# Kernel optimization log

Hardware: AMD Instinct MI355X
Metric: run time of the kernel (lower is better)

Reference implementation:

```python
import jax, jax.numpy as jnp
import numpy as np

HEADS = 16
DIM_HEAD = 64

def setup_inputs() -> dict:
    key = jax.random.key(0)
    ks = jax.random.split(key, 5)
    B, S, D = 2, 2048, 1024
    return {
        "hidden_states": jax.random.normal(ks[0], (B, S, D), dtype=jnp.float32),
        "Wq": jax.random.normal(ks[1], (D, D), dtype=jnp.float32) * (D ** -0.5),
        "Wkv": jax.random.normal(ks[2], (D, D), dtype=jnp.float32) * (D ** -0.5),
        "Wout": jax.random.normal(ks[3], (D, D), dtype=jnp.float32) * (D ** -0.5),
        "bout": jnp.zeros((D,), dtype=jnp.float32),
    }

def reference(hidden_states, Wq, Wkv, Wout, bout):
    B, S, D = hidden_states.shape
    H, Dh = HEADS, DIM_HEAD
    # projections (torch Linear: x @ W.T; here weights are stored as [in, out])
    q = hidden_states @ Wq            # [B, S, D]
    kv = hidden_states @ Wkv          # key == value share the to_kv projection
    q = q.reshape(B, S, H, Dh).transpose(0, 2, 1, 3)   # [B, H, S, Dh]
    k = kv.reshape(B, S, H, Dh).transpose(0, 2, 1, 3)
    v = k
    scale = 1.0 / np.sqrt(Dh).astype(np.float32)
    # ReLU attention: no softmax
    attn = jax.nn.relu(jnp.einsum("bhsd,bhtd->bhst", q, k) * scale)  # [B,H,S,S]
    out = jnp.einsum("bhst,bhtd->bhsd", attn, v)                     # [B,H,S,Dh]
    out = out.transpose(0, 2, 1, 3).reshape(B, S, H * Dh)
    return out @ Wout + bout
```

## Files before the change

### kernel.cpp

```cpp
#include <hip/hip_runtime.h>
#include <hip/hip_bf16.h>

#define HEADS  16
#define DIMH   64
#define NBATCH 2
#define SEQ    2048
#define DMODEL 1024
#define MROWS  (NBATCH * SEQ)

typedef __attribute__((ext_vector_type(8)))  short bf16x8;
typedef __attribute__((ext_vector_type(4)))  float f32x4;
typedef __attribute__((ext_vector_type(16))) float f32x16;
typedef __attribute__((ext_vector_type(4)))  float float4v;
typedef __attribute__((ext_vector_type(4)))  short short4v;

__device__ inline void glds16(const void* g, void* l) {
    __builtin_amdgcn_global_load_lds(
        (const __attribute__((address_space(1))) unsigned int*)g,
        (__attribute__((address_space(3))) unsigned int*)l, 16, 0, 0);
}

#define WAIT_VMCNT(N) asm volatile("s_waitcnt vmcnt(" #N ")" ::: "memory")
#define BARRIER() do { __builtin_amdgcn_s_barrier(); asm volatile("" ::: "memory"); } while (0)

__global__ void cvt_kernel(const float* __restrict__ in,
                           __hip_bfloat16* __restrict__ out, int n4) {
    int i = blockIdx.x * blockDim.x + threadIdx.x;
    if (i >= n4) return;
    float4v v = reinterpret_cast<const float4v*>(in)[i];
    union { short4v s; __hip_bfloat16 h[4]; } u;
#pragma unroll
    for (int j = 0; j < 4; ++j) u.h[j] = __float2bfloat16(v[j]);
    reinterpret_cast<short4v*>(out)[i] = u.s;
}

__global__ void combine_kernel(const float* __restrict__ p0,
                               const float* __restrict__ p1,
                               __hip_bfloat16* __restrict__ out, int n4) {
    int i = blockIdx.x * blockDim.x + threadIdx.x;
    if (i >= n4) return;
    float4v a = reinterpret_cast<const float4v*>(p0)[i];
    float4v b = reinterpret_cast<const float4v*>(p1)[i];
    union { short4v s; __hip_bfloat16 h[4]; } u;
#pragma unroll
    for (int j = 0; j < 4; ++j) u.h[j] = __float2bfloat16(a[j] + b[j]);
    reinterpret_cast<short4v*>(out)[i] = u.s;
}

__global__ void tr_kernel(const float* __restrict__ W,
                          __hip_bfloat16* __restrict__ WT) {
    __shared__ float tile[32][33];
    int i = blockIdx.y * 32 + threadIdx.y;
    int o = blockIdx.x * 32 + threadIdx.x;
    tile[threadIdx.y][threadIdx.x] = W[i * DMODEL + o];
    __syncthreads();
    int oo = blockIdx.x * 32 + threadIdx.y;
    int ii = blockIdx.y * 32 + threadIdx.x;
    WT[oo * DMODEL + ii] = __float2bfloat16(tile[threadIdx.x][threadIdx.y]);
}


__launch_bounds__(512, 2)
__global__ void proj_kernel(const __hip_bfloat16* __restrict__ hsb,
                            const __hip_bfloat16* __restrict__ WqT,
                            const __hip_bfloat16* __restrict__ WkvT,
                            __hip_bfloat16* __restrict__ qb,
                            __hip_bfloat16* __restrict__ kb,
                            __hip_bfloat16* __restrict__ vtb) {
    __shared__ __align__(16) char SLDS[73728];
    char (*Alds)[8192]  = (char (*)[8192])SLDS;
    char (*Blds)[16384] = (char (*)[16384])(SLDS + 24576);
    char* CT = SLDS;

    const int tid  = threadIdx.x;
    const int wave = tid >> 6;
    const int lane = tid & 63;
    const int lr = lane & 15;
    const int lk = lane >> 4;
    const int wm = wave >> 2, wn = wave & 3;

    int bid = blockIdx.x;
    bid = (bid & 7) * 32 + (bid >> 3);
    const int xt = bid & 7;
    const int mt = bid >> 3;
    const bool is_q = xt < 4;
    const int mbase = mt * 128;
    const int nbase = (xt & 3) * 256;
    const __hip_bfloat16* __restrict__ WT = is_q ? WqT : WkvT;

    const char* __restrict__ Ab = (const char*)(hsb + (size_t)mbase * DMODEL);
    const char* __restrict__ Bb = (const char*)(WT + (size_t)nbase * DMODEL);

    auto stage = [&](int buf, int k0) {
        const size_t colb = (size_t)k0 * 2 + lk * 16;
        glds16(Ab + (size_t)(wave * 16 + lr) * (DMODEL * 2) + colb,
               &Alds[buf][wave * 1024]);
#pragma unroll
        for (int r = 0; r < 2; ++r)
            glds16(Bb + (size_t)((r * 8 + wave) * 16 + lr) * (DMODEL * 2) + colb,
                   &Blds[buf][r * 8192 + wave * 1024]);
    };

    stage(0, 0);
    stage(1, 32);

    f32x4 acc[4][4] = {};
    int c0 = 0;
    for (int t = 0; t < DMODEL / 32; ++t) {
        if (t < DMODEL / 32 - 1) WAIT_VMCNT(3); else WAIT_VMCNT(0);
        BARRIER();
        if (t + 2 < DMODEL / 32) {
            int sb = c0 + 2; if (sb >= 3) sb -= 3;
            stage(sb, (t + 2) * 32);
        }
        bf16x8 af[4], bfr[4];
#pragma unroll
        for (int i = 0; i < 4; ++i) {
            af[i]  = *reinterpret_cast<const bf16x8*>(&Alds[c0][(wm * 4 + i) * 1024 + lane * 16]);
            bfr[i] = *reinterpret_cast<const bf16x8*>(&Blds[c0][(wn * 4 + i) * 1024 + lane * 16]);
        }
#pragma unroll
        for (int i = 0; i < 4; ++i)
#pragma unroll
            for (int j = 0; j < 4; ++j)
                acc[i][j] = __builtin_amdgcn_mfma_f32_16x16x32_bf16(af[i], bfr[j], acc[i][j], 0, 0, 0);
        c0 = (c0 + 1 == 3) ? 0 : c0 + 1;
    }

    const float qscale = is_q ? 0.125f : 1.0f;
    const int b_ = mbase >> 11;
    const int s0 = mbase & (SEQ - 1);
    BARRIER();

#pragma unroll
    for (int i = 0; i < 4; ++i)
#pragma unroll
        for (int j = 0; j < 4; ++j)
#pragma unroll
            for (int r = 0; r < 4; ++r) {
                int m = wm * 64 + i * 16 + lk * 4 + r;
                int n = wn * 64 + j * 16 + lr;
                *reinterpret_cast<__hip_bfloat16*>(
                    &CT[m * 512 + ((n * 2) ^ (((m >> 2) & 7) << 4))]) =
                    __float2bfloat16(acc[i][j][r] * qscale);
            }
    BARRIER();

    __hip_bfloat16* __restrict__ dst0 = is_q ? qb : kb;
#pragma unroll
    for (int p = 0; p < 8; ++p) {
        int g = p * 64 + (tid >> 3);
        int m = g >> 2, seg = g & 3, o = tid & 7;
        int key = ((m >> 2) & 7) << 4;
        bf16x8 val = *reinterpret_cast<const bf16x8*>(
            &CT[m * 512 + ((seg * 128 + o * 16) ^ key)]);
        int h = (nbase >> 6) + seg;
        *reinterpret_cast<bf16x8*>(
            &dst0[(((size_t)b_ * HEADS + h) * SEQ + s0 + m) * DIMH + o * 8]) = val;
    }

    if (!is_q) {
        BARRIER();
#pragma unroll
        for (int i = 0; i < 4; ++i)
#pragma unroll
            for (int j = 0; j < 4; ++j)
#pragma unroll
                for (int r = 0; r < 4; ++r) {
                    int m = wm * 64 + i * 16 + lk * 4 + r;
                    int n = wn * 64 + j * 16 + lr;
                    *reinterpret_cast<__hip_bfloat16*>(
                        &CT[n * 256 + ((m * 2) ^ ((n & 7) << 4))]) =
                        __float2bfloat16(acc[i][j][r]);
                }
        BARRIER();
#pragma unroll
        for (int p = 0; p < 8; ++p) {
            int g = p * 64 + (tid >> 3);
            int n = g >> 1, half = g & 1, o = tid & 7;
            int key2 = (n & 7) << 4;
            int D = half * 64 + o * 8;
            int mm = D >> 4, H = o & 1;
            union { unsigned long long d[2]; bf16x8 v; } val;
            val.d[0] = *reinterpret_cast<const unsigned long long*>(
                &CT[n * 256 + ((mm * 32 + H * 8) ^ key2)]);
            val.d[1] = *reinterpret_cast<const unsigned long long*>(
                &CT[n * 256 + ((mm * 32 + 16 + H * 8) ^ key2)]);
            int h = (nbase >> 6) + (n >> 6);
            int dh = n & 63;
            *reinterpret_cast<bf16x8*>(
                &vtb[(((size_t)b_ * HEADS + h) * DIMH + dh) * SEQ + s0 + D]) = val.v;
        }
    }
}

__launch_bounds__(512, 2)
__global__ void outproj_kernel(const __hip_bfloat16* __restrict__ ao,
                               const __hip_bfloat16* __restrict__ WoT,
                               const float* __restrict__ bout,
                               float* __restrict__ out) {
    __shared__ __align__(16) char Alds[3][8192];
    __shared__ __align__(16) char Blds[3][8192];
    const int tid  = threadIdx.x;
    const int wave = tid >> 6;
    const int lane = tid & 63;
    const int lr = lane & 15;
    const int lk = lane >> 4;
    const int wm = wave >> 1, wn = wave & 1;

    int bid = blockIdx.x;
    bid = (bid & 7) * 32 + (bid >> 3);
    const int xt = bid & 7;
    const int mt = bid >> 3;
    const int mbase = mt * 128;
    const int nbase = xt * 128;

    const char* __restrict__ Ab = (const char*)(ao + (size_t)mbase * DMODEL);
    const char* __restrict__ Bb = (const char*)(WoT + (size_t)nbase * DMODEL);

    auto stage = [&](int buf, int k0) {
        const size_t colb = (size_t)k0 * 2 + lk * 16;
        glds16(Ab + (size_t)(wave * 16 + lr) * (DMODEL * 2) + colb,
               &Alds[buf][wave * 1024]);
        glds16(Bb + (size_t)(wave * 16 + lr) * (DMODEL * 2) + colb,
               &Blds[buf][wave * 1024]);
    };

    stage(0, 0);
    stage(1, 32);

    f32x4 acc[2][4] = {};
    int c0 = 0;
    for (int t = 0; t < DMODEL / 32; ++t) {
        if (t < DMODEL / 32 - 1) WAIT_VMCNT(2); else WAIT_VMCNT(0);
        BARRIER();
        if (t + 2 < DMODEL / 32) {
            int sb = c0 + 2; if (sb >= 3) sb -= 3;
            stage(sb, (t + 2) * 32);
        }
        bf16x8 af[2], bfr[4];
#pragma unroll
        for (int i = 0; i < 2; ++i)
            af[i] = *reinterpret_cast<const bf16x8*>(&Alds[c0][(wm * 2 + i) * 1024 + lane * 16]);
#pragma unroll
        for (int j = 0; j < 4; ++j)
            bfr[j] = *reinterpret_cast<const bf16x8*>(&Blds[c0][(wn * 4 + j) * 1024 + lane * 16]);
#pragma unroll
        for (int i = 0; i < 2; ++i)
#pragma unroll
            for (int j = 0; j < 4; ++j)
                acc[i][j] = __builtin_amdgcn_mfma_f32_16x16x32_bf16(af[i], bfr[j], acc[i][j], 0, 0, 0);
        c0 = (c0 + 1 == 3) ? 0 : c0 + 1;
    }

#pragma unroll
    for (int j = 0; j < 4; ++j) {
        const int n = nbase + wn * 64 + j * 16 + lr;
        const float bias = bout[n];
#pragma unroll
        for (int i = 0; i < 2; ++i) {
#pragma unroll
            for (int r = 0; r < 4; ++r) {
                int m = mbase + wm * 32 + i * 16 + lk * 4 + r;
                out[(size_t)m * DMODEL + n] = acc[i][j][r] + bias;
            }
        }
    }
}

__launch_bounds__(512, 2)
__global__ void attn_kernel(const __hip_bfloat16* __restrict__ qb,
                            const __hip_bfloat16* __restrict__ kb,
                            const __hip_bfloat16* __restrict__ vtb,
                            float* __restrict__ po) {
    __shared__ __align__(16) char Klds[4][8192];
    __shared__ __align__(16) char Vlds[4][8192];
    const int lane = threadIdx.x & 63;
    const int wave = threadIdx.x >> 6;
    const int l32  = lane & 31;
    const int hi   = lane >> 5;

    int bid = blockIdx.x;
    bid = (bid & 7) * 64 + (bid >> 3);
    const int ts   = bid & 1;
    const int qblk = (bid >> 1) & 7;
    const int bh   = bid >> 4;
    const int b_ = bh >> 4, h = bh & 15;
    const int qbase = qblk * 256 + wave * 32;
    const int tbeg = ts * (SEQ / 2);

    const __hip_bfloat16* __restrict__ Q = qb + (size_t)bh * SEQ * DIMH;
    const char* __restrict__ Kg = (const char*)(kb  + (size_t)bh * SEQ * DIMH);
    const char* __restrict__ Vg = (const char*)(vtb + (size_t)bh * DIMH * SEQ);

    bf16x8 qf[4];
#pragma unroll
    for (int ks = 0; ks < 4; ++ks)
        qf[ks] = *reinterpret_cast<const bf16x8*>(
            &Q[(size_t)(qbase + l32) * DIMH + ks * 16 + hi * 8]);

    auto stage = [&](int buf, int t0) {
        glds16(Kg + (size_t)(t0 + (wave >> 2) * 32 + (lane & 31)) * 128 +
                   (wave & 3) * 32 + (lane >> 5) * 16,
               &Klds[buf][wave * 1024]);
        glds16(Vg + (size_t)((wave & 1) * 32 + (lane & 31)) * (SEQ * 2) +
                   (size_t)(t0 + (wave >> 1) * 16) * 2 + (lane >> 5) * 16,
               &Vlds[buf][wave * 1024]);
    };

    f32x16 acco[2] = {};
    f32x16 sp0, sp1;

    auto do_qk = [&](const char* Kc) {
        sp0 = f32x16{}; sp1 = f32x16{};
        __builtin_amdgcn_s_setprio(1);
#pragma unroll
        for (int ks = 0; ks < 4; ++ks) {
            bf16x8 k0f = *reinterpret_cast<const bf16x8*>(Kc + ks * 1024 + lane * 16);
            bf16x8 k1f = *reinterpret_cast<const bf16x8*>(Kc + (4 + ks) * 1024 + lane * 16);
            sp0 = __builtin_amdgcn_mfma_f32_32x32x16_bf16(k0f, qf[ks], sp0, 0, 0, 0);
            sp1 = __builtin_amdgcn_mfma_f32_32x32x16_bf16(k1f, qf[ks], sp1, 0, 0, 0);
        }
        __builtin_amdgcn_s_setprio(0);
    };

    auto do_packpv = [&](const char* Vc) {
        __builtin_amdgcn_s_setprio(1);
#pragma unroll
        for (int kt = 0; kt < 4; ++kt) {
            union { __hip_bfloat16 hh[8]; bf16x8 v; } pa;
            const int rb = (kt & 1) * 8;
#pragma unroll
            for (int j = 0; j < 8; ++j) {
                float x = (kt < 2) ? sp0[rb + j] : sp1[rb + j];
                pa.hh[j] = __float2bfloat16(fmaxf(x, 0.f));
            }
#pragma unroll
            for (int nt = 0; nt < 2; ++nt) {
                bf16x8 vbv = *reinterpret_cast<const bf16x8*>(
                    Vc + (kt * 2 + nt) * 1024 + lane * 16);
                acco[nt] = __builtin_amdgcn_mfma_f32_32x32x16_bf16(pa.v, vbv, acco[nt], 0, 0, 0);
            }
        }
        __builtin_amdgcn_s_setprio(0);
    };

    const int NT = SEQ / 2 / 64;
    stage(0, tbeg);
    stage(1, tbeg + 64);

    WAIT_VMCNT(2);
    BARRIER();
    stage(2, tbeg + 128);
    do_qk(Klds[0]);

    for (int t = 1; t < NT; ++t) {
        if (t < NT - 1) WAIT_VMCNT(2); else WAIT_VMCNT(0);
        BARRIER();
        if (t + 2 < NT) stage((t + 2) & 3, tbeg + (t + 2) * 64);
        do_packpv(Vlds[(t - 1) & 3]);
        do_qk(Klds[t & 3]);
    }
    do_packpv(Vlds[(NT - 1) & 3]);

    float* __restrict__ PO = po + (size_t)ts * MROWS * DMODEL;
#pragma unroll
    for (int nt = 0; nt < 2; ++nt) {
#pragma unroll
        for (int r = 0; r < 16; ++r) {
            int q = qbase + (r & 3) + 8 * (r >> 2) + 4 * hi;
            PO[(size_t)(b_ * SEQ + q) * DMODEL + h * 64 + nt * 32 + l32] = acco[nt][r];
        }
    }
}

extern "C" void kernel_launch(void* const* d_in, const int* in_sizes, int n_in,
                              void* d_out, int out_size, void* d_ws, size_t ws_size,
                              hipStream_t stream) {
    const float* hs   = (const float*)d_in[0];
    const float* Wq   = (const float*)d_in[1];
    const float* Wkv  = (const float*)d_in[2];
    const float* Wout = (const float*)d_in[3];
    const float* bout = (const float*)d_in[4];
    float* out = (float*)d_out;

    char* ws = (char*)d_ws;
    size_t off = 0;
    auto alloc = [&](size_t bytes) { char* p = ws + off; off += bytes; return p; };
    __hip_bfloat16* hsb  = (__hip_bfloat16*)alloc((size_t)MROWS * DMODEL * 2);
    __hip_bfloat16* WqT  = (__hip_bfloat16*)alloc((size_t)DMODEL * DMODEL * 2);
    __hip_bfloat16* WkvT = (__hip_bfloat16*)alloc((size_t)DMODEL * DMODEL * 2);
    __hip_bfloat16* WoT  = (__hip_bfloat16*)alloc((size_t)DMODEL * DMODEL * 2);
    __hip_bfloat16* qb   = (__hip_bfloat16*)alloc((size_t)MROWS * DMODEL * 2);
    __hip_bfloat16* kb   = (__hip_bfloat16*)alloc((size_t)MROWS * DMODEL * 2);
    __hip_bfloat16* vtb  = (__hip_bfloat16*)alloc((size_t)MROWS * DMODEL * 2);
    float*          po   = (float*)alloc((size_t)2 * MROWS * DMODEL * 4);
    __hip_bfloat16* ao   = hsb;

    cvt_kernel<<<(MROWS * DMODEL / 4 + 255) / 256, 256, 0, stream>>>(hs, hsb, MROWS * DMODEL / 4);
    dim3 trg(32, 32), trb(32, 32);
    tr_kernel<<<trg, trb, 0, stream>>>(Wq, WqT);
    tr_kernel<<<trg, trb, 0, stream>>>(Wkv, WkvT);
    tr_kernel<<<trg, trb, 0, stream>>>(Wout, WoT);

    proj_kernel<<<256, 512, 0, stream>>>(hsb, WqT, WkvT, qb, kb, vtb);

    attn_kernel<<<512, 512, 0, stream>>>(qb, kb, vtb, po);

    combine_kernel<<<(MROWS * DMODEL / 4 + 255) / 256, 256, 0, stream>>>(
        po, po + (size_t)MROWS * DMODEL, ao, MROWS * DMODEL / 4);

    outproj_kernel<<<256, 512, 0, stream>>>(ao, WoT, bout, out);
}
```

Measured before the change: 120.9 us.

## Double per-wave query rows in attention kernel, reuse K/V fragments across two groups

Each wave now handles 64 query rows as two 32-row groups instead of 32, so every K and V fragment read from LDS feeds twice as many MFMAs. The grid is halved to 256 blocks, each covering 512 queries. The software-pipelined split between QK and PV across iterations is removed in favour of one fused compute step per tile. This cuts LDS and global K/V traffic per FLOP, but roughly doubles accumulator register pressure, halves the number of blocks available to fill the CUs, and loses the QK/PV overlap.

```diff
diff --git a/kernel.cpp b/kernel.cpp
--- a/kernel.cpp
+++ b/kernel.cpp
@@ -281,23 +281,25 @@
     const int hi   = lane >> 5;
 
     int bid = blockIdx.x;
-    bid = (bid & 7) * 64 + (bid >> 3);
+    bid = (bid & 7) * 32 + (bid >> 3);
     const int ts   = bid & 1;
-    const int qblk = (bid >> 1) & 7;
-    const int bh   = bid >> 4;
+    const int qblk = (bid >> 1) & 3;
+    const int bh   = bid >> 3;
     const int b_ = bh >> 4, h = bh & 15;
-    const int qbase = qblk * 256 + wave * 32;
+    const int qbase = qblk * 512 + wave * 64;
     const int tbeg = ts * (SEQ / 2);
 
     const __hip_bfloat16* __restrict__ Q = qb + (size_t)bh * SEQ * DIMH;
     const char* __restrict__ Kg = (const char*)(kb  + (size_t)bh * SEQ * DIMH);
     const char* __restrict__ Vg = (const char*)(vtb + (size_t)bh * DIMH * SEQ);
 
-    bf16x8 qf[4];
-#pragma unroll
-    for (int ks = 0; ks < 4; ++ks)
-        qf[ks] = *reinterpret_cast<const bf16x8*>(
-            &Q[(size_t)(qbase + l32) * DIMH + ks * 16 + hi * 8]);
+    bf16x8 qf[2][4];
+#pragma unroll
+    for (int g = 0; g < 2; ++g)
+#pragma unroll
+        for (int ks = 0; ks < 4; ++ks)
+            qf[g][ks] = *reinterpret_cast<const bf16x8*>(
+                &Q[(size_t)(qbase + g * 32 + l32) * DIMH + ks * 16 + hi * 8]);
 
     auto stage = [&](int buf, int t0) {
         glds16(Kg + (size_t)(t0 + (wave >> 2) * 32 + (lane & 31)) * 128 +
@@ -308,38 +310,35 @@
                &Vlds[buf][wave * 1024]);
     };
 
-    f32x16 acco[2] = {};
-    f32x16 sp0, sp1;
-
-    auto do_qk = [&](const char* Kc) {
-        sp0 = f32x16{}; sp1 = f32x16{};
+    f32x16 acco[2][2] = {};
+
+    auto compute = [&](const char* Kc, const char* Vc) {
+        f32x16 sp[2][2] = {};
         __builtin_amdgcn_s_setprio(1);
 #pragma unroll
         for (int ks = 0; ks < 4; ++ks) {
             bf16x8 k0f = *reinterpret_cast<const bf16x8*>(Kc + ks * 1024 + lane * 16);
             bf16x8 k1f = *reinterpret_cast<const bf16x8*>(Kc + (4 + ks) * 1024 + lane * 16);
-            sp0 = __builtin_amdgcn_mfma_f32_32x32x16_bf16(k0f, qf[ks], sp0, 0, 0, 0);
-            sp1 = __builtin_amdgcn_mfma_f32_32x32x16_bf16(k1f, qf[ks], sp1, 0, 0, 0);
-        }
-        __builtin_amdgcn_s_setprio(0);
-    };
-
-    auto do_packpv = [&](const char* Vc) {
-        __builtin_amdgcn_s_setprio(1);
+            sp[0][0] = __builtin_amdgcn_mfma_f32_32x32x16_bf16(k0f, qf[0][ks], sp[0][0], 0, 0, 0);
+            sp[0][1] = __builtin_amdgcn_mfma_f32_32x32x16_bf16(k1f, qf[0][ks], sp[0][1], 0, 0, 0);
+            sp[1][0] = __builtin_amdgcn_mfma_f32_32x32x16_bf16(k0f, qf[1][ks], sp[1][0], 0, 0, 0);
+            sp[1][1] = __builtin_amdgcn_mfma_f32_32x32x16_bf16(k1f, qf[1][ks], sp[1][1], 0, 0, 0);
+        }
 #pragma unroll
         for (int kt = 0; kt < 4; ++kt) {
-            union { __hip_bfloat16 hh[8]; bf16x8 v; } pa;
+            bf16x8 v0 = *reinterpret_cast<const bf16x8*>(Vc + (kt * 2 + 0) * 1024 + lane * 16);
+            bf16x8 v1 = *reinterpret_cast<const bf16x8*>(Vc + (kt * 2 + 1) * 1024 + lane * 16);
             const int rb = (kt & 1) * 8;
 #pragma unroll
-            for (int j = 0; j < 8; ++j) {
-                float x = (kt < 2) ? sp0[rb + j] : sp1[rb + j];
-                pa.hh[j] = __float2bfloat16(fmaxf(x, 0.f));
-            }
-#pragma unroll
-            for (int nt = 0; nt < 2; ++nt) {
-                bf16x8 vbv = *reinterpret_cast<const bf16x8*>(
-                    Vc + (kt * 2 + nt) * 1024 + lane * 16);
-                acco[nt] = __builtin_amdgcn_mfma_f32_32x32x16_bf16(pa.v, vbv, acco[nt], 0, 0, 0);
+            for (int g = 0; g < 2; ++g) {
+                union { __hip_bfloat16 hh[8]; bf16x8 v; } pa;
+#pragma unroll
+                for (int j = 0; j < 8; ++j) {
+                    float x = (kt < 2) ? sp[g][0][rb + j] : sp[g][1][rb + j];
+                    pa.hh[j] = __float2bfloat16(fmaxf(x, 0.f));
+                }
+                acco[g][0] = __builtin_amdgcn_mfma_f32_32x32x16_bf16(pa.v, v0, acco[g][0], 0, 0, 0);
+                acco[g][1] = __builtin_amdgcn_mfma_f32_32x32x16_bf16(pa.v, v1, acco[g][1], 0, 0, 0);
             }
         }
         __builtin_amdgcn_s_setprio(0);
@@ -349,29 +348,23 @@
     stage(0, tbeg);
     stage(1, tbeg + 64);
 
-    WAIT_VMCNT(2);
-    BARRIER();
-    stage(2, tbeg + 128);
-    do_qk(Klds[0]);
-
-    for (int t = 1; t < NT; ++t) {
+    for (int t = 0; t < NT; ++t) {
         if (t < NT - 1) WAIT_VMCNT(2); else WAIT_VMCNT(0);
         BARRIER();
         if (t + 2 < NT) stage((t + 2) & 3, tbeg + (t + 2) * 64);
-        do_packpv(Vlds[(t - 1) & 3]);
-        do_qk(Klds[t & 3]);
-    }
-    do_packpv(Vlds[(NT - 1) & 3]);
+        compute(Klds[t & 3], Vlds[t & 3]);
+    }
 
     float* __restrict__ PO = po + (size_t)ts * MROWS * DMODEL;
 #pragma unroll
-    for (int nt = 0; nt < 2; ++nt) {
-#pragma unroll
-        for (int r = 0; r < 16; ++r) {
-            int q = qbase + (r & 3) + 8 * (r >> 2) + 4 * hi;
-            PO[(size_t)(b_ * SEQ + q) * DMODEL + h * 64 + nt * 32 + l32] = acco[nt][r];
-        }
-    }
+    for (int g = 0; g < 2; ++g)
+#pragma unroll
+        for (int nt = 0; nt < 2; ++nt)
+#pragma unroll
+            for (int r = 0; r < 16; ++r) {
+                int q = qbase + g * 32 + (r & 3) + 8 * (r >> 2) + 4 * hi;
+                PO[(size_t)(b_ * SEQ + q) * DMODEL + h * 64 + nt * 32 + l32] = acco[g][nt][r];
+            }
 }
 
 extern "C" void kernel_launch(void* const* d_in, const int* in_sizes, int n_in,
@@ -405,7 +398,7 @@
 
     proj_kernel<<<256, 512, 0, stream>>>(hsb, WqT, WkvT, qb, kb, vtb);
 
-    attn_kernel<<<512, 512, 0, stream>>>(qb, kb, vtb, po);
+    attn_kernel<<<256, 512, 0, stream>>>(qb, kb, vtb, po);
 
     combine_kernel<<<(MROWS * DMODEL / 4 + 255) / 256, 256, 0, stream>>>(
         po, po + (size_t)MROWS * DMODEL, ao, MROWS * DMODEL / 4);
```

Result: no change. 122.0 us (+0.9%).
